# Kernel optimization log

Hardware: AMD Instinct MI355X
Metric: run time of the kernel (lower is better)

The kernel has to match this reference:

```python
import jax, jax.numpy as jnp
import numpy as np

B, S, D, H, HD = 8, 1024, 1152, 16, 72
L, R = 32, 36  # get_decompose_dim(1152)
W_BITS, A_BITS = 4, 8


def _ste_round(x):
    return x + jax.lax.stop_gradient(jnp.round(x) - x)


def _fake_quant(x, bits):
    # symmetric fake quant, per last-dim group (per-token for acts, per-out-channel for weights)
    qmax = 2.0 ** (bits - 1) - 1.0
    scale = jnp.maximum(jnp.max(jnp.abs(x), axis=-1, keepdims=True) / qmax, 1e-8)
    return jnp.clip(_ste_round(x / scale), -qmax - 1.0, qmax) * scale


def _kron_apply(x, A, Bm):
    # DecomposeTransMatrix: x (..., L*R) -> reshape (L,R), Y = A^T X B (row-vector kron transform)
    sh = x.shape
    y = jnp.einsum('...lr,lp,rq->...pq', x.reshape(sh[:-1] + (L, R)), A, Bm)
    return y.reshape(sh)


def setup_inputs() -> dict:
    key = jax.random.key(0)
    ks = jax.random.split(key, 16)
    lin = lambda k, sh: jax.random.normal(k, sh, jnp.float32) * 0.02
    return {
        'hidden_states': jax.random.normal(ks[0], (B, S, D), jnp.float32),
        'Wq': lin(ks[1], (D, D)), 'bq': lin(ks[2], (D,)),
        'Wk': lin(ks[3], (D, D)), 'bk': lin(ks[4], (D,)),
        'Wv': lin(ks[5], (D, D)), 'bv': lin(ks[6], (D,)),
        'Wo': lin(ks[7], (D, D)), 'bo': lin(ks[8], (D,)),
        'ln_A': jnp.eye(L, dtype=jnp.float32) + 0.02 * jax.random.normal(ks[9], (L, L), jnp.float32),
        'ln_B': jnp.eye(R, dtype=jnp.float32) + 0.02 * jax.random.normal(ks[10], (R, R), jnp.float32),
        'ln_diag': 1.0 + 0.1 * jax.random.uniform(ks[11], (D,), jnp.float32),
        'vc': jnp.eye(HD, dtype=jnp.float32) + 0.02 * jax.random.normal(ks[12], (HD, HD), jnp.float32),
        'o_mat': jnp.eye(H, dtype=jnp.float32) + 0.02 * jax.random.normal(ks[13], (H, H), jnp.float32),
    }


def reference(hidden_states, Wq, bq, Wk, bk, Wv, bv, Wo, bo, ln_A, ln_B, ln_diag, vc, o_mat):
    invA_T = jnp.linalg.inv(ln_A).T
    invB_T = jnp.linalg.inv(ln_B).T
    # ln_trans applied to activations (diag scale + decomposed Kronecker rotation)
    x = _kron_apply(hidden_states * ln_diag, ln_A, ln_B)  # (B,S,D)

    def qlinear(xin, W, b, out_vc=None):
        # qa_trans inv_t folded into weight: W' = kron(W/diag, invA.T, invB.T) over input dim
        Wt = _kron_apply(W * (1.0 / ln_diag), invA_T, invB_T)
        bt = b
        if out_vc is not None:  # vc_trans folded into to_v output channels
            Wt = jnp.einsum('hdi,de->hei', Wt.reshape(H, HD, D), out_vc).reshape(D, D)
            bt = (b.reshape(H, HD) @ out_vc).reshape(-1)
        return _fake_quant(xin, A_BITS) @ _fake_quant(Wt, W_BITS).T + bt

    q = qlinear(x, Wq, bq).reshape(B, S, H, HD).transpose(0, 2, 1, 3)  # (B,H,S,HD)
    k = qlinear(x, Wk, bk).reshape(B, S, H, HD).transpose(0, 2, 1, 3)
    v = qlinear(x, Wv, bv, out_vc=vc).reshape(B, S, H, HD).transpose(0, 2, 1, 3)

    # baddbmm with beta=0, alpha=1: NO 1/sqrt(d) scaling (faithful to source)
    scores = jnp.einsum('bhqd,bhkd->bhqk', q, k)
    attn = jax.nn.softmax(scores.astype(jnp.float32), axis=-1).astype(q.dtype)
    ctx = jnp.einsum('bhqk,bhkd->bhqd', attn, v).transpose(0, 2, 1, 3)  # (B,S,H,HD)

    # o_trans: matmul(o_mat.T, Y) per token
    ctx = jnp.einsum('bsgd,gh->bshd', ctx, o_mat).reshape(B, S, D)

    # to_out with qa_trans=[inv(O).T, inv(V).T] folded into weight
    o_it = jnp.linalg.inv(o_mat).T
    v_it = jnp.linalg.inv(vc).T
    Wot = jnp.einsum('gh,ogd,de->ohe', o_it, Wo.reshape(D, H, HD), v_it).reshape(D, D)
    out = _fake_quant(ctx, A_BITS) @ _fake_quant(Wot, W_BITS).T + bo
    return out  # rescale_output_factor = 1.0
```

## Files before the change

kernel.cpp:

```cpp
#include <hip/hip_runtime.h>
#include <hip/hip_bf16.h>

#define BB 8
#define SS 1024
#define DD 1152
#define HH 16
#define HD 72
#define PD 96
#define LL 32
#define RR 36
#define NTOK (BB*SS)

typedef __attribute__((ext_vector_type(8)))  short short8;
typedef __attribute__((ext_vector_type(4)))  float f32x4;
typedef __attribute__((ext_vector_type(16))) float f32x16;
typedef __attribute__((ext_vector_type(4)))  unsigned short ushort4v;

#define F_IAT   0
#define F_IBT   1024
#define F_IO    2320
#define F_IV    2576
#define F_BVT   7760
#define F_SX    16384
#define F_SWQ   24576
#define F_SWK   25728
#define F_SWV   26880
#define F_SWO   28032
#define F_SCTX  32768
#define B_R1    1048576ULL
#define B_WB    (B_R1 + 37748736ULL)
#define B_XB    (B_WB + 4ULL*2654208ULL)
#define B_QB    (B_XB + 18874368ULL)
#define B_KB    (B_QB + 25165824ULL)
#define B_VB    (B_KB + 25165824ULL)
#define B_VT    (B_VB + 25165824ULL)
#define WSLOT   1327104ULL

__device__ __forceinline__ unsigned bf16rne(float f) {
    unsigned u = __builtin_bit_cast(unsigned, f);
    return (u + 0x7fffu + ((u >> 16) & 1u)) >> 16;
}
__device__ __forceinline__ unsigned cvtpk(float lo, float hi) {
    unsigned r;
    asm("v_cvt_pk_bf16_f32 %0, %1, %2" : "=v"(r) : "v"(lo), "v"(hi));
    return r;
}
__device__ __forceinline__ short8 mk8(unsigned a, unsigned b, unsigned c, unsigned d) {
    union { unsigned u[4]; short8 s; } t;
    t.u[0] = a; t.u[1] = b; t.u[2] = c; t.u[3] = d;
    return t.s;
}
__device__ __forceinline__ void async_ld16(void* lds, const void* g) {
    __builtin_amdgcn_global_load_lds((const __attribute__((address_space(1))) unsigned*)g,
                                     (__attribute__((address_space(3))) unsigned*)lds, 16, 0, 0);
}

__global__ __launch_bounds__(128) void invert_kernel(const float* __restrict__ A32, const float* __restrict__ B36,
                                                     const float* __restrict__ O16, const float* __restrict__ V72,
                                                     float* __restrict__ ws)
{
    __shared__ float As[80*76], Xs[80*76], Ys[80*76], Ps[80*76], Wt[80*76];
    int which = blockIdx.x;
    int n; const float* src;
    if (which == 0)      { n = 32; src = A32; }
    else if (which == 1) { n = 36; src = B36; }
    else if (which == 2) { n = 16; src = O16; }
    else                 { n = 72; src = V72; }
    int tid = threadIdx.x;
    int nq = n >> 2;
    for (int idx = tid; idx < n*n; idx += 128) {
        int i = idx / n, j = idx % n;
        float a = src[idx];
        As[i*76 + j] = a;
        Xs[i*76 + j] = (i == j ? 2.0f : 0.0f) - a;
    }
    __syncthreads();
    int ty = tid >> 3, qq = tid & 7;

#define NSGEMM(DST, SA, SB) { \
    f32x4 c00={0,0,0,0},c01={0,0,0,0},c02={0,0,0,0}, \
          c10={0,0,0,0},c11={0,0,0,0},c12={0,0,0,0}, \
          c20={0,0,0,0},c21={0,0,0,0},c22={0,0,0,0}, \
          c30={0,0,0,0},c31={0,0,0,0},c32={0,0,0,0}, \
          c40={0,0,0,0},c41={0,0,0,0},c42={0,0,0,0}; \
    _Pragma("unroll 2") \
    for (int k = 0; k < n; ++k) { \
        const float* sb = &SB[k*76]; \
        f32x4 b0 = *(const f32x4*)(sb + 4*qq); \
        f32x4 b1 = *(const f32x4*)(sb + 4*qq + 32); \
        f32x4 b2 = *(const f32x4*)(sb + 4*qq + 64); \
        float a0 = SA[ty*76 + k]; \
        float a1 = SA[(ty+16)*76 + k]; \
        float a2 = SA[(ty+32)*76 + k]; \
        float a3 = SA[(ty+48)*76 + k]; \
        float a4 = SA[(ty+64)*76 + k]; \
        c00 += a0*b0; c01 += a0*b1; c02 += a0*b2; \
        c10 += a1*b0; c11 += a1*b1; c12 += a1*b2; \
        c20 += a2*b0; c21 += a2*b1; c22 += a2*b2; \
        c30 += a3*b0; c31 += a3*b1; c32 += a3*b2; \
        c40 += a4*b0; c41 += a4*b1; c42 += a4*b2; \
    } \
    { \
        f32x4 cc[5][3] = {{c00,c01,c02},{c10,c11,c12},{c20,c21,c22},{c30,c31,c32},{c40,c41,c42}}; \
        _Pragma("unroll") \
        for (int m = 0; m < 5; ++m) { \
            int i = ty + 16*m; \
            if (i < n) { \
                _Pragma("unroll") \
                for (int c = 0; c < 3; ++c) { \
                    int q = qq + 8*c; \
                    if (q < nq) *(f32x4*)&DST[i*76 + 4*q] = cc[m][c]; \
                } \
            } \
        } \
    } \
}
#define NSELEM(P_, Y_) { \
    for (int idx = tid; idx < n*n; idx += 128) { \
        int i = idx / n, j = idx % n; \
        P_[i*76 + j] = P_[i*76 + j] - 3.0f*Y_[i*76 + j] + (i == j ? 3.0f : 0.0f); \
    } \
}
    float* Xc = Xs;
    float* Xn = Wt;
    for (int it = 0; it < 3; ++it) {
        NSGEMM(Ys, As, Xc); __syncthreads();
        NSGEMM(Ps, Ys, Ys); __syncthreads();
        NSELEM(Ps, Ys);     __syncthreads();
        NSGEMM(Xn, Xc, Ps); __syncthreads();
        float* t = Xc; Xc = Xn; Xn = t;
    }
#undef NSGEMM
#undef NSELEM
    if (which == 0) {
        for (int idx = tid; idx < 32*32; idx += 128) { int l = idx/32, pp = idx%32; ws[F_IAT + idx] = Xc[pp*76 + l]; }
    } else if (which == 1) {
        for (int idx = tid; idx < 36*36; idx += 128) { int r = idx/36, qx = idx%36; ws[F_IBT + idx] = Xc[qx*76 + r]; }
    } else if (which == 2) {
        for (int idx = tid; idx < 16*16; idx += 128) { int i = idx/16, j = idx%16; ws[F_IO + idx] = Xc[i*76 + j]; }
    } else {
        for (int idx = tid; idx < 72*72; idx += 128) { int i = idx/72, j = idx%72; ws[F_IV + idx] = Xc[i*76 + j]; }
    }
}

__global__ __launch_bounds__(256) void kron_act_q(const float* __restrict__ src, unsigned short* __restrict__ dst,
                                                  float* __restrict__ scl,
                                                  const float* __restrict__ P, const float* __restrict__ Q,
                                                  const float* __restrict__ diag)
{
    __shared__ float Xs[LL*RR], T1[LL*RR], Ps[LL*LL], Qs[RR*RR], Ys[LL*RR], red[256];
    int row = blockIdx.x;
    int tid = threadIdx.x;
    const float* sr = src + (size_t)row*DD;
    for (int i = tid; i < LL*LL; i += 256) Ps[i] = P[i];
    for (int i = tid; i < RR*RR; i += 256) Qs[i] = Q[i];
    for (int i = tid; i < DD; i += 256) Xs[i] = sr[i]*diag[i];
    __syncthreads();
    for (int s = tid; s < 288; s += 256) {
        int p = s / 9, r4 = (s % 9)*4;
        f32x4 acc = {0.f,0.f,0.f,0.f};
        #pragma unroll 8
        for (int l = 0; l < LL; ++l) {
            float a = Ps[l*LL + p];
            f32x4 x = *(const f32x4*)&Xs[l*RR + r4];
            acc += a*x;
        }
        *(f32x4*)&T1[p*RR + r4] = acc;
    }
    __syncthreads();
    float lmax = 0.f;
    for (int s = tid; s < 288; s += 256) {
        int p = s / 9, q4 = (s % 9)*4;
        f32x4 acc = {0.f,0.f,0.f,0.f};
        #pragma unroll 9
        for (int r = 0; r < RR; ++r) {
            float t = T1[p*RR + r];
            f32x4 qv = *(const f32x4*)&Qs[r*RR + q4];
            acc += t*qv;
        }
        *(f32x4*)&Ys[p*RR + q4] = acc;
        lmax = fmaxf(lmax, fmaxf(fmaxf(fabsf(acc[0]), fabsf(acc[1])), fmaxf(fabsf(acc[2]), fabsf(acc[3]))));
    }
    red[tid] = lmax; __syncthreads();
    for (int s = 128; s > 0; s >>= 1) { if (tid < s) red[tid] = fmaxf(red[tid], red[tid+s]); __syncthreads(); }
    float scale = fmaxf(red[0]/127.f, 1e-8f);
    float rs = 1.f/scale;
    if (tid == 0) scl[row] = scale;
    for (int s = tid; s < 288; s += 256) {
        int i4 = s*4;
        f32x4 y = *(const f32x4*)&Ys[i4];
        ushort4v o;
        #pragma unroll
        for (int c = 0; c < 4; ++c) {
            float v = rintf(y[c]*rs);
            v = fminf(fmaxf(v, -128.f), 127.f);
            o[c] = (unsigned short)bf16rne(v);
        }
        *(ushort4v*)&dst[(size_t)row*DD + i4] = o;
    }
}

__global__ __launch_bounds__(256) void kron_w_q(const float* __restrict__ src, unsigned short* __restrict__ dst,
                                                float* __restrict__ scl,
                                                const float* __restrict__ P, const float* __restrict__ Q,
                                                const float* __restrict__ diag)
{
    __shared__ float Xs[LL*RR], T1[LL*RR], Ps[LL*LL], Qs[RR*RR], Ys[LL*RR], red[256];
    int row = blockIdx.x;
    int tid = threadIdx.x;
    const float* sr = src + (size_t)row*DD;
    for (int i = tid; i < LL*LL; i += 256) Ps[i] = P[i];
    for (int i = tid; i < RR*RR; i += 256) Qs[i] = Q[i];
    for (int i = tid; i < DD; i += 256) Xs[i] = sr[i]*(1.0f/diag[i]);
    __syncthreads();
    for (int s = tid; s < 288; s += 256) {
        int p = s / 9, r4 = (s % 9)*4;
        f32x4 acc = {0.f,0.f,0.f,0.f};
        #pragma unroll 8
        for (int l = 0; l < LL; ++l) {
            float a = Ps[l*LL + p];
            f32x4 x = *(const f32x4*)&Xs[l*RR + r4];
            acc += a*x;
        }
        *(f32x4*)&T1[p*RR + r4] = acc;
    }
    __syncthreads();
    float lmax = 0.f;
    for (int s = tid; s < 288; s += 256) {
        int p = s / 9, q4 = (s % 9)*4;
        f32x4 acc = {0.f,0.f,0.f,0.f};
        #pragma unroll 9
        for (int r = 0; r < RR; ++r) {
            float t = T1[p*RR + r];
            f32x4 qv = *(const f32x4*)&Qs[r*RR + q4];
            acc += t*qv;
        }
        *(f32x4*)&Ys[p*RR + q4] = acc;
        lmax = fmaxf(lmax, fmaxf(fmaxf(fabsf(acc[0]), fabsf(acc[1])), fmaxf(fabsf(acc[2]), fabsf(acc[3]))));
    }
    red[tid] = lmax; __syncthreads();
    for (int s = 128; s > 0; s >>= 1) { if (tid < s) red[tid] = fmaxf(red[tid], red[tid+s]); __syncthreads(); }
    float scale = fmaxf(red[0]/7.f, 1e-8f);
    float rs = 1.f/scale;
    if (tid == 0) scl[row] = scale;
    for (int s = tid; s < 288; s += 256) {
        int i4 = s*4;
        f32x4 y = *(const f32x4*)&Ys[i4];
        ushort4v o;
        #pragma unroll
        for (int c = 0; c < 4; ++c) {
            float v = rintf(y[c]*rs);
            v = fminf(fmaxf(v, -8.f), 7.f);
            o[c] = (unsigned short)bf16rne(v);
        }
        *(ushort4v*)&dst[(size_t)row*DD + i4] = o;
    }
}

__global__ __launch_bounds__(256) void kron_rows(const float* __restrict__ src, float* __restrict__ dst,
                                                 const float* __restrict__ P, const float* __restrict__ Q,
                                                 const float* __restrict__ diag)
{
    __shared__ float Xs[LL*RR], T1[LL*RR], Ps[LL*LL], Qs[RR*RR];
    int row = blockIdx.x;
    int tid = threadIdx.x;
    const float* sr = src + (size_t)row*DD;
    for (int i = tid; i < LL*LL; i += 256) Ps[i] = P[i];
    for (int i = tid; i < RR*RR; i += 256) Qs[i] = Q[i];
    for (int i = tid; i < DD; i += 256) Xs[i] = sr[i]*(1.0f/diag[i]);
    __syncthreads();
    for (int s = tid; s < 288; s += 256) {
        int p = s / 9, r4 = (s % 9)*4;
        f32x4 acc = {0.f,0.f,0.f,0.f};
        #pragma unroll 8
        for (int l = 0; l < LL; ++l) {
            float a = Ps[l*LL + p];
            f32x4 x = *(const f32x4*)&Xs[l*RR + r4];
            acc += a*x;
        }
        *(f32x4*)&T1[p*RR + r4] = acc;
    }
    __syncthreads();
    for (int s = tid; s < 288; s += 256) {
        int p = s / 9, q4 = (s % 9)*4;
        f32x4 acc = {0.f,0.f,0.f,0.f};
        #pragma unroll 9
        for (int r = 0; r < RR; ++r) {
            float t = T1[p*RR + r];
            f32x4 qv = *(const f32x4*)&Qs[r*RR + q4];
            acc += t*qv;
        }
        *(f32x4*)&dst[(size_t)row*DD + p*RR + q4] = acc;
    }
}

__global__ __launch_bounds__(256) void wv_fold_q(const float* __restrict__ tmp, const float* __restrict__ vc,
                                                 const float* __restrict__ bv, unsigned short* __restrict__ dst,
                                                 float* __restrict__ scl, float* __restrict__ bvt)
{
    int he = blockIdx.x;
    int h = he / HD, e = he % HD;
    __shared__ float vcol[HD], Ys[DD], red[256];
    int tid = threadIdx.x;
    if (tid < HD) vcol[tid] = vc[tid*HD + e];
    __syncthreads();
    const float* base = tmp + (size_t)h*HD*DD;
    float lmax = 0.f;
    for (int i = tid; i < DD; i += 256) {
        float acc = 0.f;
        #pragma unroll 8
        for (int d = 0; d < HD; ++d) acc += base[(size_t)d*DD + i]*vcol[d];
        Ys[i] = acc;
        lmax = fmaxf(lmax, fabsf(acc));
    }
    red[tid] = lmax; __syncthreads();
    for (int s = 128; s > 0; s >>= 1) { if (tid < s) red[tid] = fmaxf(red[tid], red[tid+s]); __syncthreads(); }
    float scale = fmaxf(red[0]/7.f, 1e-8f);
    float rs = 1.f/scale;
    if (tid == 0) {
        scl[he] = scale;
        float acc = 0.f;
        for (int d = 0; d < HD; ++d) acc += bv[h*HD + d]*vcol[d];
        bvt[he] = acc;
    }
    for (int i = tid; i < DD; i += 256) {
        float v = rintf(Ys[i]*rs);
        v = fminf(fmaxf(v, -8.f), 7.f);
        dst[(size_t)he*DD + i] = (unsigned short)bf16rne(v);
    }
}

__global__ __launch_bounds__(256) void wo_trans_q(const float* __restrict__ Wo, const float* __restrict__ iO,
                                                  const float* __restrict__ iV, unsigned short* __restrict__ dst,
                                                  float* __restrict__ scl)
{
    __shared__ float M[HH*HD], T1[HH*HD], iOs[HH*HH], iVs[HD*HD], Ys[DD], red[256];
    int row = blockIdx.x, tid = threadIdx.x;
    for (int i = tid; i < DD; i += 256) M[i] = Wo[(size_t)row*DD + i];
    for (int i = tid; i < HH*HH; i += 256) iOs[i] = iO[i];
    for (int i = tid; i < HD*HD; i += 256) iVs[i] = iV[i];
    __syncthreads();
    for (int i = tid; i < DD; i += 256) {
        int h = i / HD, d = i % HD;
        float a = 0.f;
        #pragma unroll
        for (int g = 0; g < HH; ++g) a += iOs[h*HH + g]*M[g*HD + d];
        T1[i] = a;
    }
    __syncthreads();
    float lmax = 0.f;
    for (int i = tid; i < DD; i += 256) {
        int h = i / HD, e = i % HD;
        float a = 0.f;
        #pragma unroll 8
        for (int d = 0; d < HD; ++d) a += T1[h*HD + d]*iVs[e*HD + d];
        Ys[i] = a;
        lmax = fmaxf(lmax, fabsf(a));
    }
    red[tid] = lmax; __syncthreads();
    for (int s = 128; s > 0; s >>= 1) { if (tid < s) red[tid] = fmaxf(red[tid], red[tid+s]); __syncthreads(); }
    float scale = fmaxf(red[0]/7.f, 1e-8f);
    float rs = 1.f/scale;
    if (tid == 0) scl[row] = scale;
    for (int i = tid; i < DD; i += 256) {
        float v = rintf(Ys[i]*rs);
        v = fminf(fmaxf(v, -8.f), 7.f);
        dst[(size_t)row*DD + i] = (unsigned short)bf16rne(v);
    }
}

__device__ __forceinline__ void gemm_body(const unsigned short* __restrict__ Xb, const unsigned short* __restrict__ Wb,
                                          unsigned short* As, unsigned short* Bs, f32x4 (&acc)[4][4],
                                          int wr, int wc, int lr, int lg)
{
    for (int k0 = 0; k0 < DD; k0 += 32) {
        int tid = threadIdx.x;
        #pragma unroll
        for (int j = 0; j < 2; ++j) {
            int idx = tid + j*256;
            int row = idx >> 2, pp = idx & 3;
            int s = pp ^ ((row >> 1) & 3);
            async_ld16(&As[idx*8], Xb + (size_t)row*DD + k0 + s*8);
            async_ld16(&Bs[idx*8], Wb + (size_t)row*DD + k0 + s*8);
        }
        __syncthreads();
        short8 a[4], bfr[4];
        #pragma unroll
        for (int fr = 0; fr < 4; ++fr) {
            int row = wr*64 + fr*16 + lr;
            a[fr] = *(const short8*)(&As[row*32 + (lg ^ ((row>>1)&3))*8]);
        }
        #pragma unroll
        for (int fc = 0; fc < 4; ++fc) {
            int row = wc*64 + fc*16 + lr;
            bfr[fc] = *(const short8*)(&Bs[row*32 + (lg ^ ((row>>1)&3))*8]);
        }
        #pragma unroll
        for (int fr = 0; fr < 4; ++fr)
            #pragma unroll
            for (int fc = 0; fc < 4; ++fc)
                acc[fr][fc] = __builtin_amdgcn_mfma_f32_16x16x32_bf16(a[fr], bfr[fc], acc[fr][fc], 0, 0, 0);
        __syncthreads();
    }
}

__global__ __launch_bounds__(256) void gemm_qkv(const unsigned short* __restrict__ X,
                                                const unsigned short* __restrict__ Wq_b,
                                                const unsigned short* __restrict__ Wk_b,
                                                const unsigned short* __restrict__ Wv_b,
                                                const float* __restrict__ sx, const float* __restrict__ ws_all,
                                                const float* __restrict__ bq, const float* __restrict__ bk,
                                                const float* __restrict__ bvt,
                                                unsigned short* __restrict__ qb, unsigned short* __restrict__ kb,
                                                unsigned short* __restrict__ vb)
{
    __shared__ unsigned short smem[8192];
    unsigned short* As = smem;
    unsigned short* Bs = smem + 4096;
    int lin = blockIdx.x;
    int nl = (lin & 7)*216 + (lin >> 3);
    int z = nl / 576;
    int rem = nl - z*576;
    int bm = rem / 9, bn = rem - bm*9;
    const unsigned short* W = (z == 0) ? Wq_b : (z == 1) ? Wk_b : Wv_b;
    const float* sw_ = ws_all + (size_t)z*1152;
    const float* bias = (z == 0) ? bq : (z == 1) ? bk : bvt;
    unsigned short* outQ = (z == 0) ? qb : (z == 1) ? kb : vb;
    int tid = threadIdx.x;
    int wave = tid >> 6, lane = tid & 63;
    int wr = wave >> 1, wc = wave & 1;
    int lr = lane & 15, lg = lane >> 4;
    f32x4 acc[4][4];
    #pragma unroll
    for (int i = 0; i < 4; ++i)
        #pragma unroll
        for (int j = 0; j < 4; ++j)
            #pragma unroll
            for (int e = 0; e < 4; ++e) acc[i][j][e] = 0.f;
    gemm_body(X + (size_t)bm*128*DD, W + (size_t)bn*128*DD, As, Bs, acc, wr, wc, lr, lg);
    float swn[4], bnv[4];
    #pragma unroll
    for (int fc = 0; fc < 4; ++fc) {
        int n = bn*128 + wc*64 + fc*16 + lr;
        swn[fc] = sw_[n]; bnv[fc] = bias[n];
    }
    #pragma unroll
    for (int c = 0; c < 2; ++c) {
        __syncthreads();
        if (wr == c) {
            #pragma unroll
            for (int fr = 0; fr < 4; ++fr) {
                #pragma unroll
                for (int j = 0; j < 4; ++j) {
                    int rloc = fr*16 + lg*4 + j;
                    float sxm = sx[bm*128 + c*64 + rloc];
                    #pragma unroll
                    for (int fc = 0; fc < 4; ++fc) {
                        int cloc = wc*64 + fc*16 + lr;
                        float v = acc[fr][fc][j]*sxm*swn[fc] + bnv[fc];
                        smem[rloc*128 + cloc] = (unsigned short)bf16rne(v);
                    }
                }
            }
        }
        __syncthreads();
        #pragma unroll
        for (int it = 0; it < 4; ++it) {
            int idx = tid + it*256;
            int row = idx >> 4, seg = idx & 15;
            size_t g = ((size_t)(bm*128 + c*64 + row))*DD + bn*128 + seg*8;
            *(short8*)(&outQ[g]) = *(const short8*)(&smem[row*128 + seg*8]);
        }
    }
}

__global__ __launch_bounds__(256) void gemm_out(const unsigned short* __restrict__ X, const unsigned short* __restrict__ W,
                                                const float* __restrict__ sx, const float* __restrict__ sw_,
                                                const float* __restrict__ bias, float* __restrict__ outF)
{
    __shared__ unsigned short As[128*32];
    __shared__ unsigned short Bs[128*32];
    int lin = blockIdx.x;
    int nl = (lin & 7)*72 + (lin >> 3);
    int bm = nl / 9, bn = nl - bm*9;
    int tid = threadIdx.x;
    int wave = tid >> 6, lane = tid & 63;
    int wr = wave >> 1, wc = wave & 1;
    int lr = lane & 15, lg = lane >> 4;
    f32x4 acc[4][4];
    #pragma unroll
    for (int i = 0; i < 4; ++i)
        #pragma unroll
        for (int j = 0; j < 4; ++j)
            #pragma unroll
            for (int e = 0; e < 4; ++e) acc[i][j][e] = 0.f;
    gemm_body(X + (size_t)bm*128*DD, W + (size_t)bn*128*DD, As, Bs, acc, wr, wc, lr, lg);
    #pragma unroll
    for (int fc = 0; fc < 4; ++fc) {
        int n = bn*128 + wc*64 + fc*16 + lr;
        float swn = sw_[n], bnv = bias[n];
        #pragma unroll
        for (int fr = 0; fr < 4; ++fr) {
            #pragma unroll
            for (int j = 0; j < 4; ++j) {
                int mrow = bm*128 + wr*64 + fr*16 + lg*4 + j;
                outF[(size_t)mrow*DD + n] = acc[fr][fc][j]*sx[mrow]*swn + bnv;
            }
        }
    }
}

__global__ __launch_bounds__(256) void transpose_v(const unsigned short* __restrict__ v, unsigned short* __restrict__ vT)
{
    __shared__ unsigned short t[64][100];
    int head = blockIdx.x >> 4, st = blockIdx.x & 15;
    int b = head >> 4, h = head & 15;
    int tid = threadIdx.x;
    const unsigned short* src = v + ((size_t)(b*SS + st*64))*DD + h*HD;
    for (int idx = tid; idx < 64*PD; idx += 256) {
        int i = idx / PD, d = idx % PD;
        t[i][d] = (d < HD) ? src[(size_t)i*DD + d] : (unsigned short)0;
    }
    __syncthreads();
    unsigned short* dst = vT + (size_t)head*PD*SS + st*64;
    for (int idx = tid; idx < PD*64; idx += 256) {
        int d = idx >> 6, i = idx & 63;
        dst[(size_t)d*SS + i] = t[i][d];
    }
}

__global__ __launch_bounds__(256) void attn_mfma(const unsigned short* __restrict__ q, const unsigned short* __restrict__ k,
                                                 const unsigned short* __restrict__ vT, float* __restrict__ ctx)
{
    __shared__ unsigned short Kl[64*128];
    __shared__ unsigned short Vl[96*64];
    int lin = blockIdx.x;
    int nl = (lin & 7)*128 + (lin >> 3);
    int bh = nl >> 3;
    int qblk = nl & 7;
    int tid = threadIdx.x;
    int wave = tid >> 6, lane = tid & 63;
    int lq = lane & 31, half = lane >> 5;
    int b = bh >> 4, h = bh & 15;
    const unsigned short* qrow = q + ((size_t)(b*SS + qblk*128 + wave*32 + lq))*DD + h*HD;
    const unsigned short* kbb  = k + (size_t)b*SS*DD + h*HD;
    const unsigned short* vtb  = vT + (size_t)bh*PD*SS;
    short8 zero8 = {0,0,0,0,0,0,0,0};
    short8 qf[6];
    #pragma unroll
    for (int ks = 0; ks < 4; ++ks)
        qf[ks] = *(const short8*)(qrow + ks*16 + half*8);
    qf[4] = (half == 0) ? *(const short8*)(qrow + 64) : zero8;
    qf[5] = zero8;
    f32x16 O0, O1, O2;
    #pragma unroll
    for (int r = 0; r < 16; ++r) { O0[r] = 0.f; O1[r] = 0.f; O2[r] = 0.f; }
    float m = -1e30f, l = 0.f;
    for (int t0 = 0; t0 < SS; t0 += 64) {
        __syncthreads();
        #pragma unroll
        for (int j = 0; j < 3; ++j) {
            int idx = tid + j*256;
            int row = idx / 12, s = idx % 12;
            int phys = s ^ (row & 7);
            short8 val = zero8;
            if (s < 9) val = *(const short8*)(kbb + (size_t)(t0 + row)*DD + s*8);
            *(short8*)(&Kl[row*128 + phys*8]) = val;
        }
        #pragma unroll
        for (int j = 0; j < 3; ++j) {
            int idx = tid + j*256;
            int d = idx >> 3, p = idx & 7;
            int s = p ^ (d & 7);
            short8 val = *(const short8*)(vtb + (size_t)d*SS + t0 + s*8);
            *(short8*)(&Vl[d*64 + p*8]) = val;
        }
        __syncthreads();
        #pragma unroll
        for (int sub = 0; sub < 2; ++sub) {
            f32x16 sacc;
            #pragma unroll
            for (int r = 0; r < 16; ++r) sacc[r] = 0.f;
            __builtin_amdgcn_s_setprio(1);
            #pragma unroll
            for (int ks = 0; ks < 6; ++ks) {
                int key = sub*32 + lq;
                short8 kf = *(const short8*)(&Kl[key*128 + (((ks*2 + half) ^ (lq & 7)))*8]);
                sacc = __builtin_amdgcn_mfma_f32_32x32x16_bf16(kf, qf[ks], sacc, 0, 0, 0);
            }
            __builtin_amdgcn_s_setprio(0);
            float pa = fmaxf(fmaxf(sacc[0], sacc[1]), fmaxf(sacc[2], sacc[3]));
            float pb = fmaxf(fmaxf(sacc[4], sacc[5]), fmaxf(sacc[6], sacc[7]));
            float pc = fmaxf(fmaxf(sacc[8], sacc[9]), fmaxf(sacc[10], sacc[11]));
            float pd = fmaxf(fmaxf(sacc[12], sacc[13]), fmaxf(sacc[14], sacc[15]));
            float pmax = fmaxf(fmaxf(pa, pb), fmaxf(pc, pd));
            pmax = fmaxf(pmax, __shfl_xor(pmax, 32));
            if (!__all(pmax - m <= 8.0f)) {
                float mn = fmaxf(m, pmax);
                float corr = __expf(m - mn);
                m = mn;
                l *= corr;
                #pragma unroll
                for (int r = 0; r < 16; ++r) {
                    int rowq = (r&3) + 8*(r>>2) + 4*half;
                    float cr = __shfl(corr, rowq);
                    O0[r] *= cr; O1[r] *= cr; O2[r] *= cr;
                }
            }
            float p[16]; float ls = 0.f;
            #pragma unroll
            for (int r = 0; r < 16; ++r) { p[r] = __expf(sacc[r] - m); ls += p[r]; }
            ls += __shfl_xor(ls, 32);
            l += ls;
            unsigned pk[8], sw[8];
            #pragma unroll
            for (int j2 = 0; j2 < 8; ++j2) pk[j2] = cvtpk(p[2*j2], p[2*j2+1]);
            #pragma unroll
            for (int j2 = 0; j2 < 8; ++j2) sw[j2] = __shfl_xor(pk[j2], 32);
            short8 A0 = half ? mk8(sw[2], sw[3], pk[2], pk[3]) : mk8(pk[0], pk[1], sw[0], sw[1]);
            short8 A1 = half ? mk8(sw[6], sw[7], pk[6], pk[7]) : mk8(pk[4], pk[5], sw[4], sw[5]);
            __builtin_amdgcn_s_setprio(1);
            #pragma unroll
            for (int dt = 0; dt < 3; ++dt) {
                int d = dt*32 + lq;
                short8 vf0 = *(const short8*)(&Vl[d*64 + (((sub*4 + half) ^ (d & 7)))*8]);
                short8 vf1 = *(const short8*)(&Vl[d*64 + (((sub*4 + 2 + half) ^ (d & 7)))*8]);
                if (dt == 0) { O0 = __builtin_amdgcn_mfma_f32_32x32x16_bf16(A0, vf0, O0, 0,0,0);
                               O0 = __builtin_amdgcn_mfma_f32_32x32x16_bf16(A1, vf1, O0, 0,0,0); }
                if (dt == 1) { O1 = __builtin_amdgcn_mfma_f32_32x32x16_bf16(A0, vf0, O1, 0,0,0);
                               O1 = __builtin_amdgcn_mfma_f32_32x32x16_bf16(A1, vf1, O1, 0,0,0); }
                if (dt == 2) { O2 = __builtin_amdgcn_mfma_f32_32x32x16_bf16(A0, vf0, O2, 0,0,0);
                               O2 = __builtin_amdgcn_mfma_f32_32x32x16_bf16(A1, vf1, O2, 0,0,0); }
            }
            __builtin_amdgcn_s_setprio(0);
        }
    }
    float linv = 1.f / l;
    #pragma unroll
    for (int r = 0; r < 16; ++r) {
        int rowq = (r&3) + 8*(r>>2) + 4*half;
        float lr2 = __shfl(linv, rowq);
        int s = qblk*128 + wave*32 + rowq;
        size_t base = ((size_t)(b*SS + s))*DD + h*HD;
        ctx[base + lq]      = O0[r]*lr2;
        ctx[base + 32 + lq] = O1[r]*lr2;
        if (lq < 8) ctx[base + 64 + lq] = O2[r]*lr2;
    }
}

__global__ __launch_bounds__(256) void octx_fq_q(const float* __restrict__ ctx, const float* __restrict__ o_mat,
                                                 unsigned short* __restrict__ out, float* __restrict__ scl)
{
    __shared__ float ct[DD], Ys[DD], om[HH*HH], red[256];
    int t = blockIdx.x, tid = threadIdx.x;
    for (int i = tid; i < DD; i += 256) ct[i] = ctx[(size_t)t*DD + i];
    for (int i = tid; i < HH*HH; i += 256) om[i] = o_mat[i];
    __syncthreads();
    float lmax = 0.f;
    for (int s = tid; s < 288; s += 256) {
        int h = s / 18, d4 = (s % 18)*4;
        f32x4 acc = {0.f,0.f,0.f,0.f};
        #pragma unroll
        for (int g = 0; g < HH; ++g) {
            float o = om[g*HH + h];
            f32x4 c = *(const f32x4*)&ct[g*HD + d4];
            acc += o*c;
        }
        *(f32x4*)&Ys[h*HD + d4] = acc;
        lmax = fmaxf(lmax, fmaxf(fmaxf(fabsf(acc[0]), fabsf(acc[1])), fmaxf(fabsf(acc[2]), fabsf(acc[3]))));
    }
    red[tid] = lmax; __syncthreads();
    for (int s = 128; s > 0; s >>= 1) { if (tid < s) red[tid] = fmaxf(red[tid], red[tid+s]); __syncthreads(); }
    float scale = fmaxf(red[0]/127.f, 1e-8f);
    float rs = 1.f/scale;
    if (tid == 0) scl[t] = scale;
    for (int s = tid; s < 288; s += 256) {
        int i4 = s*4;
        f32x4 y = *(const f32x4*)&Ys[i4];
        ushort4v o;
        #pragma unroll
        for (int c = 0; c < 4; ++c) {
            float v = rintf(y[c]*rs);
            v = fminf(fmaxf(v, -128.f), 127.f);
            o[c] = (unsigned short)bf16rne(v);
        }
        *(ushort4v*)&out[(size_t)t*DD + i4] = o;
    }
}

extern "C" void kernel_launch(void* const* d_in, const int* in_sizes, int n_in,
                              void* d_out, int out_size, void* d_ws, size_t ws_size,
                              hipStream_t stream)
{
    const float* hidden = (const float*)d_in[0];
    const float* Wq = (const float*)d_in[1];  const float* bq = (const float*)d_in[2];
    const float* Wk = (const float*)d_in[3];  const float* bk = (const float*)d_in[4];
    const float* Wv = (const float*)d_in[5];  const float* bv = (const float*)d_in[6];
    const float* Wo = (const float*)d_in[7];  const float* bo = (const float*)d_in[8];
    const float* lnA = (const float*)d_in[9];
    const float* lnB = (const float*)d_in[10];
    const float* ln_diag = (const float*)d_in[11];
    const float* vc = (const float*)d_in[12];
    const float* o_mat = (const float*)d_in[13];
    float* ws = (float*)d_ws;
    float* out = (float*)d_out;
    char* wsb = (char*)d_ws;

    float* iAT  = ws + F_IAT;
    float* iBT  = ws + F_IBT;
    float* iO   = ws + F_IO;
    float* iV   = ws + F_IV;
    float* bvt  = ws + F_BVT;
    float* s_x  = ws + F_SX;
    float* s_wq = ws + F_SWQ;
    float* s_wk = ws + F_SWK;
    float* s_wv = ws + F_SWV;
    float* s_wo = ws + F_SWO;
    float* s_ct = ws + F_SCTX;

    float* slot = (float*)(wsb + B_R1);
    float* Wvm  = slot + 2*WSLOT;
    float* ctxf = slot;

    unsigned short* Wq_b = (unsigned short*)(wsb + B_WB);
    unsigned short* Wk_b = Wq_b + WSLOT;
    unsigned short* Wv_b = Wq_b + 2*WSLOT;
    unsigned short* Wo_b = Wq_b + 3*WSLOT;
    unsigned short* x_b  = (unsigned short*)(wsb + B_XB);
    unsigned short* ctx_b = x_b;
    unsigned short* qb = (unsigned short*)(wsb + B_QB);
    unsigned short* kb = (unsigned short*)(wsb + B_KB);
    unsigned short* vb = (unsigned short*)(wsb + B_VB);
    unsigned short* vT = (unsigned short*)(wsb + B_VT);

    invert_kernel<<<4, 128, 0, stream>>>(lnA, lnB, o_mat, vc, ws);
    kron_act_q<<<NTOK, 256, 0, stream>>>(hidden, x_b, s_x, lnA, lnB, ln_diag);
    kron_w_q<<<DD, 256, 0, stream>>>(Wq, Wq_b, s_wq, iAT, iBT, ln_diag);
    kron_w_q<<<DD, 256, 0, stream>>>(Wk, Wk_b, s_wk, iAT, iBT, ln_diag);
    kron_rows<<<DD, 256, 0, stream>>>(Wv, Wvm, iAT, iBT, ln_diag);
    wv_fold_q<<<DD, 256, 0, stream>>>(Wvm, vc, bv, Wv_b, s_wv, bvt);
    wo_trans_q<<<DD, 256, 0, stream>>>(Wo, iO, iV, Wo_b, s_wo);
    gemm_qkv<<<dim3(1728), 256, 0, stream>>>(x_b, Wq_b, Wk_b, Wv_b, s_x, s_wq, bq, bk, bvt, qb, kb, vb);
    transpose_v<<<BB*HH*16, 256, 0, stream>>>(vb, vT);
    attn_mfma<<<dim3(1024), 256, 0, stream>>>(qb, kb, vT, ctxf);
    octx_fq_q<<<NTOK, 256, 0, stream>>>(ctxf, o_mat, ctx_b, s_ct);
    gemm_out<<<dim3(576), 256, 0, stream>>>(ctx_b, Wo_b, s_ct, s_wo, bo, out);
}
```

Baseline: 620.5 us.

## Double-buffer GEMM loads, fuse V transpose into QKV epilogue, merge weight kron launches

GEMM main loops now prefetch the next K-slice into a second LDS buffer with async loads, overlapping global loads with MFMA work. The QKV GEMM writes V directly in transposed per-head layout, removing the separate transpose kernel and its extra global traffic. The three weight kron transforms are merged into one launch, and attention zero-fills the K/V padding once instead of per tile. This doubles LDS use per block, which may reduce occupancy, and the transposed V stores are less coalesced.

```diff
diff --git a/kernel.cpp b/kernel.cpp
--- a/kernel.cpp
+++ b/kernel.cpp
@@ -200,13 +200,18 @@
     }
 }
 
-__global__ __launch_bounds__(256) void kron_w_q(const float* __restrict__ src, unsigned short* __restrict__ dst,
-                                                float* __restrict__ scl,
-                                                const float* __restrict__ P, const float* __restrict__ Q,
-                                                const float* __restrict__ diag)
+__global__ __launch_bounds__(256) void kron_w3(const float* __restrict__ Wq, const float* __restrict__ Wk,
+                                               const float* __restrict__ Wv,
+                                               unsigned short* __restrict__ Wq_b, unsigned short* __restrict__ Wk_b,
+                                               float* __restrict__ Wvm,
+                                               float* __restrict__ s_wq, float* __restrict__ s_wk,
+                                               const float* __restrict__ P, const float* __restrict__ Q,
+                                               const float* __restrict__ diag)
 {
     __shared__ float Xs[LL*RR], T1[LL*RR], Ps[LL*LL], Qs[RR*RR], Ys[LL*RR], red[256];
-    int row = blockIdx.x;
+    int z = blockIdx.x / DD;
+    int row = blockIdx.x % DD;
+    const float* src = (z == 0) ? Wq : (z == 1) ? Wk : Wv;
     int tid = threadIdx.x;
     const float* sr = src + (size_t)row*DD;
     for (int i = tid; i < LL*LL; i += 256) Ps[i] = P[i];
@@ -238,10 +243,20 @@
         *(f32x4*)&Ys[p*RR + q4] = acc;
         lmax = fmaxf(lmax, fmaxf(fmaxf(fabsf(acc[0]), fabsf(acc[1])), fmaxf(fabsf(acc[2]), fabsf(acc[3]))));
     }
+    if (z == 2) {
+        __syncthreads();
+        for (int s = tid; s < 288; s += 256) {
+            int i4 = s*4;
+            *(f32x4*)&Wvm[(size_t)row*DD + i4] = *(const f32x4*)&Ys[i4];
+        }
+        return;
+    }
     red[tid] = lmax; __syncthreads();
     for (int s = 128; s > 0; s >>= 1) { if (tid < s) red[tid] = fmaxf(red[tid], red[tid+s]); __syncthreads(); }
     float scale = fmaxf(red[0]/7.f, 1e-8f);
     float rs = 1.f/scale;
+    float* scl = (z == 0) ? s_wq : s_wk;
+    unsigned short* dst = (z == 0) ? Wq_b : Wk_b;
     if (tid == 0) scl[row] = scale;
     for (int s = tid; s < 288; s += 256) {
         int i4 = s*4;
@@ -254,43 +269,6 @@
             o[c] = (unsigned short)bf16rne(v);
         }
         *(ushort4v*)&dst[(size_t)row*DD + i4] = o;
-    }
-}
-
-__global__ __launch_bounds__(256) void kron_rows(const float* __restrict__ src, float* __restrict__ dst,
-                                                 const float* __restrict__ P, const float* __restrict__ Q,
-                                                 const float* __restrict__ diag)
-{
-    __shared__ float Xs[LL*RR], T1[LL*RR], Ps[LL*LL], Qs[RR*RR];
-    int row = blockIdx.x;
-    int tid = threadIdx.x;
-    const float* sr = src + (size_t)row*DD;
-    for (int i = tid; i < LL*LL; i += 256) Ps[i] = P[i];
-    for (int i = tid; i < RR*RR; i += 256) Qs[i] = Q[i];
-    for (int i = tid; i < DD; i += 256) Xs[i] = sr[i]*(1.0f/diag[i]);
-    __syncthreads();
-    for (int s = tid; s < 288; s += 256) {
-        int p = s / 9, r4 = (s % 9)*4;
-        f32x4 acc = {0.f,0.f,0.f,0.f};
-        #pragma unroll 8
-        for (int l = 0; l < LL; ++l) {
-            float a = Ps[l*LL + p];
-            f32x4 x = *(const f32x4*)&Xs[l*RR + r4];
-            acc += a*x;
-        }
-        *(f32x4*)&T1[p*RR + r4] = acc;
-    }
-    __syncthreads();
-    for (int s = tid; s < 288; s += 256) {
-        int p = s / 9, q4 = (s % 9)*4;
-        f32x4 acc = {0.f,0.f,0.f,0.f};
-        #pragma unroll 9
-        for (int r = 0; r < RR; ++r) {
-            float t = T1[p*RR + r];
-            f32x4 qv = *(const f32x4*)&Qs[r*RR + q4];
-            acc += t*qv;
-        }
-        *(f32x4*)&dst[(size_t)row*DD + p*RR + q4] = acc;
     }
 }
 
@@ -369,38 +347,51 @@
     }
 }
 
-__device__ __forceinline__ void gemm_body(const unsigned short* __restrict__ Xb, const unsigned short* __restrict__ Wb,
-                                          unsigned short* As, unsigned short* Bs, f32x4 (&acc)[4][4],
-                                          int wr, int wc, int lr, int lg)
-{
-    for (int k0 = 0; k0 < DD; k0 += 32) {
-        int tid = threadIdx.x;
-        #pragma unroll
-        for (int j = 0; j < 2; ++j) {
-            int idx = tid + j*256;
-            int row = idx >> 2, pp = idx & 3;
-            int s = pp ^ ((row >> 1) & 3);
-            async_ld16(&As[idx*8], Xb + (size_t)row*DD + k0 + s*8);
-            async_ld16(&Bs[idx*8], Wb + (size_t)row*DD + k0 + s*8);
-        }
-        __syncthreads();
+#define GEMM_STAGE(As, Bs, bufo, k0_, Xb, Wb, tid) { \
+    _Pragma("unroll") for (int j_ = 0; j_ < 2; ++j_) { \
+        int idx_ = (tid) + j_*256; \
+        int row_ = idx_ >> 2, pp_ = idx_ & 3; \
+        int s_ = pp_ ^ ((row_ >> 1) & 3); \
+        async_ld16(&As[(bufo) + idx_*8], (Xb) + (size_t)row_*DD + (k0_) + s_*8); \
+        async_ld16(&Bs[(bufo) + idx_*8], (Wb) + (size_t)row_*DD + (k0_) + s_*8); \
+    } }
+
+__device__ __forceinline__ void gemm_body_db(const unsigned short* __restrict__ Xb, const unsigned short* __restrict__ Wb,
+                                             unsigned short* As, unsigned short* Bs, f32x4 (&acc)[4][4],
+                                             int wr, int wc, int lr, int lg)
+{
+    int tid = threadIdx.x;
+    GEMM_STAGE(As, Bs, 0, 0, Xb, Wb, tid);
+    int cur = 0;
+    for (int t = 0; t < 36; ++t) {
+        if (t < 35) {
+            GEMM_STAGE(As, Bs, (cur^1)*4096, (t+1)*32, Xb, Wb, tid);
+            asm volatile("s_waitcnt vmcnt(4)" ::: "memory");
+        } else {
+            asm volatile("s_waitcnt vmcnt(0)" ::: "memory");
+        }
+        __builtin_amdgcn_sched_barrier(0);
+        __builtin_amdgcn_s_barrier();
+        const unsigned short* Ab = &As[cur*4096];
+        const unsigned short* Bb = &Bs[cur*4096];
         short8 a[4], bfr[4];
         #pragma unroll
         for (int fr = 0; fr < 4; ++fr) {
             int row = wr*64 + fr*16 + lr;
-            a[fr] = *(const short8*)(&As[row*32 + (lg ^ ((row>>1)&3))*8]);
+            a[fr] = *(const short8*)(&Ab[row*32 + (lg ^ ((row>>1)&3))*8]);
         }
         #pragma unroll
         for (int fc = 0; fc < 4; ++fc) {
             int row = wc*64 + fc*16 + lr;
-            bfr[fc] = *(const short8*)(&Bs[row*32 + (lg ^ ((row>>1)&3))*8]);
+            bfr[fc] = *(const short8*)(&Bb[row*32 + (lg ^ ((row>>1)&3))*8]);
         }
         #pragma unroll
         for (int fr = 0; fr < 4; ++fr)
             #pragma unroll
             for (int fc = 0; fc < 4; ++fc)
                 acc[fr][fc] = __builtin_amdgcn_mfma_f32_16x16x32_bf16(a[fr], bfr[fc], acc[fr][fc], 0, 0, 0);
-        __syncthreads();
+        __builtin_amdgcn_s_barrier();
+        cur ^= 1;
     }
 }
 
@@ -412,11 +403,11 @@
                                                 const float* __restrict__ bq, const float* __restrict__ bk,
                                                 const float* __restrict__ bvt,
                                                 unsigned short* __restrict__ qb, unsigned short* __restrict__ kb,
-                                                unsigned short* __restrict__ vb)
-{
-    __shared__ unsigned short smem[8192];
+                                                unsigned short* __restrict__ vT)
+{
+    __shared__ __align__(16) unsigned short smem[16384];
     unsigned short* As = smem;
-    unsigned short* Bs = smem + 4096;
+    unsigned short* Bs = smem + 8192;
     int lin = blockIdx.x;
     int nl = (lin & 7)*216 + (lin >> 3);
     int z = nl / 576;
@@ -425,7 +416,6 @@
     const unsigned short* W = (z == 0) ? Wq_b : (z == 1) ? Wk_b : Wv_b;
     const float* sw_ = ws_all + (size_t)z*1152;
     const float* bias = (z == 0) ? bq : (z == 1) ? bk : bvt;
-    unsigned short* outQ = (z == 0) ? qb : (z == 1) ? kb : vb;
     int tid = threadIdx.x;
     int wave = tid >> 6, lane = tid & 63;
     int wr = wave >> 1, wc = wave & 1;
@@ -437,39 +427,78 @@
         for (int j = 0; j < 4; ++j)
             #pragma unroll
             for (int e = 0; e < 4; ++e) acc[i][j][e] = 0.f;
-    gemm_body(X + (size_t)bm*128*DD, W + (size_t)bn*128*DD, As, Bs, acc, wr, wc, lr, lg);
+    gemm_body_db(X + (size_t)bm*128*DD, W + (size_t)bn*128*DD, As, Bs, acc, wr, wc, lr, lg);
     float swn[4], bnv[4];
     #pragma unroll
     for (int fc = 0; fc < 4; ++fc) {
         int n = bn*128 + wc*64 + fc*16 + lr;
         swn[fc] = sw_[n]; bnv[fc] = bias[n];
     }
-    #pragma unroll
-    for (int c = 0; c < 2; ++c) {
-        __syncthreads();
-        if (wr == c) {
-            #pragma unroll
-            for (int fr = 0; fr < 4; ++fr) {
+    if (z <= 1) {
+        unsigned short* outQ = (z == 0) ? qb : kb;
+        #pragma unroll
+        for (int c = 0; c < 2; ++c) {
+            __syncthreads();
+            if (wr == c) {
                 #pragma unroll
-                for (int j = 0; j < 4; ++j) {
-                    int rloc = fr*16 + lg*4 + j;
-                    float sxm = sx[bm*128 + c*64 + rloc];
+                for (int fr = 0; fr < 4; ++fr) {
                     #pragma unroll
-                    for (int fc = 0; fc < 4; ++fc) {
-                        int cloc = wc*64 + fc*16 + lr;
-                        float v = acc[fr][fc][j]*sxm*swn[fc] + bnv[fc];
-                        smem[rloc*128 + cloc] = (unsigned short)bf16rne(v);
+                    for (int j = 0; j < 4; ++j) {
+                        int rloc = fr*16 + lg*4 + j;
+                        float sxm = sx[bm*128 + c*64 + rloc];
+                        #pragma unroll
+                        for (int fc = 0; fc < 4; ++fc) {
+                            int cloc = wc*64 + fc*16 + lr;
+                            float v = acc[fr][fc][j]*sxm*swn[fc] + bnv[fc];
+                            smem[rloc*128 + cloc] = (unsigned short)bf16rne(v);
+                        }
                     }
                 }
             }
-        }
-        __syncthreads();
-        #pragma unroll
-        for (int it = 0; it < 4; ++it) {
-            int idx = tid + it*256;
-            int row = idx >> 4, seg = idx & 15;
-            size_t g = ((size_t)(bm*128 + c*64 + row))*DD + bn*128 + seg*8;
-            *(short8*)(&outQ[g]) = *(const short8*)(&smem[row*128 + seg*8]);
+            __syncthreads();
+            #pragma unroll
+            for (int it = 0; it < 4; ++it) {
+                int idx = tid + it*256;
+                int row = idx >> 4, seg = idx & 15;
+                size_t g = ((size_t)(bm*128 + c*64 + row))*DD + bn*128 + seg*8;
+                *(short8*)(&outQ[g]) = *(const short8*)(&smem[row*128 + seg*8]);
+            }
+        }
+    } else {
+        int b = bm >> 3;
+        int srow = (bm & 7)*128;
+        #pragma unroll
+        for (int c = 0; c < 2; ++c) {
+            __syncthreads();
+            if (wr == c) {
+                #pragma unroll
+                for (int fr = 0; fr < 4; ++fr) {
+                    #pragma unroll
+                    for (int j = 0; j < 4; ++j) {
+                        int rloc = fr*16 + lg*4 + j;
+                        float sxm = sx[bm*128 + c*64 + rloc];
+                        #pragma unroll
+                        for (int fc = 0; fc < 4; ++fc) {
+                            int cloc = wc*64 + fc*16 + lr;
+                            float v = acc[fr][fc][j]*sxm*swn[fc] + bnv[fc];
+                            smem[rloc*130 + cloc] = (unsigned short)bf16rne(v);
+                        }
+                    }
+                }
+            }
+            __syncthreads();
+            #pragma unroll
+            for (int it = 0; it < 4; ++it) {
+                int idx = tid + it*256;
+                int tok8 = idx & 7, cloc = idx >> 3;
+                int n = bn*128 + cloc;
+                int h = n / 72, hd = n - h*72;
+                unsigned short tmp[8];
+                #pragma unroll
+                for (int kk = 0; kk < 8; ++kk) tmp[kk] = smem[(tok8*8 + kk)*130 + cloc];
+                size_t g = ((size_t)((b*HH + h)*PD + hd))*SS + srow + c*64 + tok8*8;
+                *(short8*)(&vT[g]) = *(const short8*)tmp;
+            }
         }
     }
 }
@@ -478,8 +507,9 @@
                                                 const float* __restrict__ sx, const float* __restrict__ sw_,
                                                 const float* __restrict__ bias, float* __restrict__ outF)
 {
-    __shared__ unsigned short As[128*32];
-    __shared__ unsigned short Bs[128*32];
+    __shared__ __align__(16) unsigned short smem[16384];
+    unsigned short* As = smem;
+    unsigned short* Bs = smem + 8192;
     int lin = blockIdx.x;
     int nl = (lin & 7)*72 + (lin >> 3);
     int bm = nl / 9, bn = nl - bm*9;
@@ -494,7 +524,7 @@
         for (int j = 0; j < 4; ++j)
             #pragma unroll
             for (int e = 0; e < 4; ++e) acc[i][j][e] = 0.f;
-    gemm_body(X + (size_t)bm*128*DD, W + (size_t)bn*128*DD, As, Bs, acc, wr, wc, lr, lg);
+    gemm_body_db(X + (size_t)bm*128*DD, W + (size_t)bn*128*DD, As, Bs, acc, wr, wc, lr, lg);
     #pragma unroll
     for (int fc = 0; fc < 4; ++fc) {
         int n = bn*128 + wc*64 + fc*16 + lr;
@@ -507,25 +537,6 @@
                 outF[(size_t)mrow*DD + n] = acc[fr][fc][j]*sx[mrow]*swn + bnv;
             }
         }
-    }
-}
-
-__global__ __launch_bounds__(256) void transpose_v(const unsigned short* __restrict__ v, unsigned short* __restrict__ vT)
-{
-    __shared__ unsigned short t[64][100];
-    int head = blockIdx.x >> 4, st = blockIdx.x & 15;
-    int b = head >> 4, h = head & 15;
-    int tid = threadIdx.x;
-    const unsigned short* src = v + ((size_t)(b*SS + st*64))*DD + h*HD;
-    for (int idx = tid; idx < 64*PD; idx += 256) {
-        int i = idx / PD, d = idx % PD;
-        t[i][d] = (d < HD) ? src[(size_t)i*DD + d] : (unsigned short)0;
-    }
-    __syncthreads();
-    unsigned short* dst = vT + (size_t)head*PD*SS + st*64;
-    for (int idx = tid; idx < PD*64; idx += 256) {
-        int d = idx >> 6, i = idx & 63;
-        dst[(size_t)d*SS + i] = t[i][d];
     }
 }
 
@@ -552,24 +563,26 @@
         qf[ks] = *(const short8*)(qrow + ks*16 + half*8);
     qf[4] = (half == 0) ? *(const short8*)(qrow + 64) : zero8;
     qf[5] = zero8;
+    for (int idx = tid; idx < 192; idx += 256) {
+        int row = idx / 3, s = 9 + idx % 3;
+        *(short8*)(&Kl[row*128 + (s ^ (row & 7))*8]) = zero8;
+    }
+    for (int idx = tid; idx < 192; idx += 256) {
+        int d = 72 + (idx >> 3), p = idx & 7;
+        *(short8*)(&Vl[d*64 + p*8]) = zero8;
+    }
     f32x16 O0, O1, O2;
     #pragma unroll
     for (int r = 0; r < 16; ++r) { O0[r] = 0.f; O1[r] = 0.f; O2[r] = 0.f; }
     float m = -1e30f, l = 0.f;
     for (int t0 = 0; t0 < SS; t0 += 64) {
         __syncthreads();
-        #pragma unroll
-        for (int j = 0; j < 3; ++j) {
-            int idx = tid + j*256;
-            int row = idx / 12, s = idx % 12;
-            int phys = s ^ (row & 7);
-            short8 val = zero8;
-            if (s < 9) val = *(const short8*)(kbb + (size_t)(t0 + row)*DD + s*8);
-            *(short8*)(&Kl[row*128 + phys*8]) = val;
-        }
-        #pragma unroll
-        for (int j = 0; j < 3; ++j) {
-            int idx = tid + j*256;
+        for (int idx = tid; idx < 576; idx += 256) {
+            int row = idx / 9, s = idx % 9;
+            short8 val = *(const short8*)(kbb + (size_t)(t0 + row)*DD + s*8);
+            *(short8*)(&Kl[row*128 + (s ^ (row & 7))*8]) = val;
+        }
+        for (int idx = tid; idx < 576; idx += 256) {
             int d = idx >> 3, p = idx & 7;
             int s = p ^ (d & 7);
             short8 val = *(const short8*)(vtb + (size_t)d*SS + t0 + s*8);
@@ -730,18 +743,14 @@
     unsigned short* ctx_b = x_b;
     unsigned short* qb = (unsigned short*)(wsb + B_QB);
     unsigned short* kb = (unsigned short*)(wsb + B_KB);
-    unsigned short* vb = (unsigned short*)(wsb + B_VB);
     unsigned short* vT = (unsigned short*)(wsb + B_VT);
 
     invert_kernel<<<4, 128, 0, stream>>>(lnA, lnB, o_mat, vc, ws);
     kron_act_q<<<NTOK, 256, 0, stream>>>(hidden, x_b, s_x, lnA, lnB, ln_diag);
-    kron_w_q<<<DD, 256, 0, stream>>>(Wq, Wq_b, s_wq, iAT, iBT, ln_diag);
-    kron_w_q<<<DD, 256, 0, stream>>>(Wk, Wk_b, s_wk, iAT, iBT, ln_diag);
-    kron_rows<<<DD, 256, 0, stream>>>(Wv, Wvm, iAT, iBT, ln_diag);
+    kron_w3<<<3*DD, 256, 0, stream>>>(Wq, Wk, Wv, Wq_b, Wk_b, Wvm, s_wq, s_wk, iAT, iBT, ln_diag);
     wv_fold_q<<<DD, 256, 0, stream>>>(Wvm, vc, bv, Wv_b, s_wv, bvt);
     wo_trans_q<<<DD, 256, 0, stream>>>(Wo, iO, iV, Wo_b, s_wo);
-    gemm_qkv<<<dim3(1728), 256, 0, stream>>>(x_b, Wq_b, Wk_b, Wv_b, s_x, s_wq, bq, bk, bvt, qb, kb, vb);
-    transpose_v<<<BB*HH*16, 256, 0, stream>>>(vb, vT);
+    gemm_qkv<<<dim3(1728), 256, 0, stream>>>(x_b, Wq_b, Wk_b, Wv_b, s_x, s_wq, bq, bk, bvt, qb, kb, vT);
     attn_mfma<<<dim3(1024), 256, 0, stream>>>(qb, kb, vT, ctxf);
     octx_fq_q<<<NTOK, 256, 0, stream>>>(ctxf, o_mat, ctx_b, s_ct);
     gemm_out<<<dim3(576), 256, 0, stream>>>(ctx_b, Wo_b, s_ct, s_wo, bo, out);
```

Result: faster. 597.1 us (-3.8%).
